# Performance work log

Hardware: AMD Instinct MI355X
Metric: run time of the kernel (lower is better)

Reference implementation:

```python
import jax, jax.numpy as jnp
import numpy as np

B, N, W = 4, 16384, 4          # batch, npoints, point feature width (xyz + intensity)
M, K = 512, 32                  # nsample keypoints, neighbors per keypoint
DIL = 2.0
NK = int(K * DIL)               # dilated candidate pool
KG = 8                          # knn size inside DGCNN edge-convs
C3 = 256


def _fps(xyz, m):
    """Farthest point sampling. xyz: (B,N,3) -> indices (B,m)."""
    Bb, Nn, _ = xyz.shape
    def step(carry, _):
        mind, cur = carry
        p = jnp.take_along_axis(xyz, cur[:, None, None], axis=1)  # (B,1,3)
        d = jnp.sum((xyz - p) ** 2, axis=-1)                       # (B,N)
        mind = jnp.minimum(mind, d)
        nxt = jnp.argmax(mind, axis=-1).astype(jnp.int32)
        return (mind, nxt), cur
    init = (jnp.full((Bb, Nn), 1e10, xyz.dtype), jnp.zeros((Bb,), jnp.int32))
    _, idx = jax.lax.scan(step, init, None, length=m)
    return jnp.transpose(idx)  # (B,m)


def _edge_conv(x, w, g, b, kg):
    """Dynamic-graph edge conv. x: (G,P,C) -> (G,P,D). Feature = cat(x_j-x_i, x_i)."""
    sq = jnp.sum(x * x, axis=-1)
    d2 = sq[:, :, None] + sq[:, None, :] - 2.0 * jnp.einsum('gpc,gqc->gpq', x, x)
    _, idx = jax.lax.top_k(-d2, kg)                                   # (G,P,kg)
    xj = jnp.take_along_axis(x[:, None], idx[..., None], axis=2)      # (G,P,kg,C)
    ef = jnp.concatenate([xj - x[:, :, None, :],
                          jnp.broadcast_to(x[:, :, None, :], xj.shape)], axis=-1)
    h = jnp.einsum('gpkc,cd->gpkd', ef, w)
    h = jax.nn.relu(g * h + b)  # BN (inference, unit running stats) + ReLU
    return jnp.max(h, axis=2)   # max over graph neighbors


def setup_inputs() -> dict:
    key = jax.random.key(0)
    ks = jax.random.split(key, 12)
    s = 0.05
    inp = {
        'x': jax.random.normal(ks[0], (B, N, W), jnp.float32),
        'rand_idx': jax.random.randint(ks[1], (K,), 0, NK),
        # DGCNN edge-conv params
        'w_e1': jax.random.normal(ks[2], (24, 64), jnp.float32) * s,
        'g1': jnp.ones((64,), jnp.float32), 'b1': jnp.zeros((64,), jnp.float32),
        'w_e2': jax.random.normal(ks[3], (128, C3), jnp.float32) * s,
        'g2': jnp.ones((C3,), jnp.float32), 'b2': jnp.zeros((C3,), jnp.float32),
        # saliency MLP (1x1 conv1d stacks)
        'w_m1': jax.random.normal(ks[4], (C3, C3), jnp.float32) * s,
        'bm1': jnp.zeros((C3,), jnp.float32),
        'gm1': jnp.ones((C3,), jnp.float32), 'bbm1': jnp.zeros((C3,), jnp.float32),
        'w_m2': jax.random.normal(ks[5], (C3, C3), jnp.float32) * s,
        'bm2': jnp.zeros((C3,), jnp.float32),
        'gm2': jnp.ones((C3,), jnp.float32), 'bbm2': jnp.zeros((C3,), jnp.float32),
        'w_m3': jax.random.normal(ks[6], (C3, 1), jnp.float32) * s,
        'bm3': jnp.zeros((1,), jnp.float32),
    }
    return inp


def reference(x, rand_idx, w_e1, g1, b1, w_e2, g2, b2,
              w_m1, bm1, gm1, bbm1, w_m2, bm2, gm2, bbm2, w_m3, bm3):
    rand_idx = rand_idx.astype(jnp.int32)
    # ---- FPS keypoint sampling ----
    node_idx = _fps(x[:, :, :3], M)                                   # (B,M)
    node = jnp.take_along_axis(x, node_idx[:, :, None], axis=1)       # (B,M,W)
    # ---- random dilation encoding: nk-NN then random k of them ----
    nxyz, pxyz = node[:, :, :3], x[:, :, :3]
    d2 = (jnp.sum(nxyz * nxyz, -1)[:, :, None] + jnp.sum(pxyz * pxyz, -1)[:, None, :]
          - 2.0 * jnp.einsum('bmc,bnc->bmn', nxyz, pxyz))             # (B,M,N)
    _, nn = jax.lax.top_k(-d2, NK)                                    # (B,M,NK)
    sel = nn[:, :, rand_idx]                                          # (B,M,K)
    neigh = jnp.take_along_axis(x[:, None], sel[..., None], axis=2)   # (B,M,K,W)
    rel = neigh[..., :3] - nxyz[:, :, None, :]
    dist = jnp.linalg.norm(rel, axis=-1, keepdims=True)
    node_rep = jnp.broadcast_to(node[:, :, None, :], neigh.shape)
    cluster = jnp.concatenate([node_rep, neigh, rel, dist], axis=-1)  # (B,M,K,12)
    random_cluster = jnp.transpose(cluster, (0, 3, 1, 2))             # (B,12,M,K)
    random_xyz = neigh[..., :3]                                       # (B,M,K,3)
    # ---- DGCNN embedding per cluster ----
    g = cluster.reshape(B * M, K, 12)
    h = _edge_conv(g, w_e1, g1, b1, KG)                               # (BM,K,64)
    h = _edge_conv(h, w_e2, g2, b2, KG)                               # (BM,K,256)
    emb = jnp.transpose(h.reshape(B, M, K, C3), (0, 3, 1, 2))         # (B,256,M,K)
    # ---- attention-weighted pooling ----
    x1 = jnp.max(emb, axis=1)                                         # (B,M,K)
    aw = jax.nn.softmax(x1, axis=-1)
    keypoints = jnp.einsum('bmk,bmkc->bcm', aw, random_xyz)           # (B,3,M)
    afm = emb * aw[:, None]                                           # (B,256,M,K)
    gcf = jnp.sum(afm, axis=-1)                                       # (B,256,M)
    # ---- saliency uncertainty MLP ----
    h = jax.nn.relu(gm1[None, :, None] * (jnp.einsum('bcm,cd->bdm', gcf, w_m1)
                                          + bm1[None, :, None]) + bbm1[None, :, None])
    h = jax.nn.relu(gm2[None, :, None] * (jnp.einsum('bcm,cd->bdm', h, w_m2)
                                          + bm2[None, :, None]) + bbm2[None, :, None])
    s = jnp.einsum('bcm,cd->bdm', h, w_m3) + bm3[None, :, None]       # (B,1,M)
    sal = jax.nn.softplus(s)[:, 0, :] + 0.001                         # (B,M)
    return keypoints, sal, random_cluster, afm
```

## Files before the change

### kernel.cpp

```cpp
#include <hip/hip_runtime.h>
#include <cstdint>

#define Bn 4
#define Nn 16384
#define Mn 512
#define Kn 32

#define O_SAL 6144
#define O_RC  8192
#define O_AFM 794624

__device__ __forceinline__ unsigned fkey(float f) {
  unsigned b = __float_as_uint(f);
  return (b & 0x80000000u) ? ~b : (b | 0x80000000u);
}

__device__ __forceinline__ unsigned long long dkey(double d) {
  unsigned long long b = (unsigned long long)__double_as_longlong(d);
  return (b & 0x8000000000000000ull) ? ~b : (b | 0x8000000000000000ull);
}

__global__ __launch_bounds__(256) void sq_kernel(const float* __restrict__ x,
                                                 float* __restrict__ sqp) {
#pragma clang fp contract(off)
  int i = blockIdx.x * 256 + threadIdx.x;
  float4 v = ((const float4*)x)[i];
  float qx = v.x * v.x;
  float qy = v.y * v.y;
  float qz = v.z * v.z;
  sqp[i] = (qx + qy) + qz;
}

template <int CTRL>
__device__ __forceinline__ float dppmaxf(float v) {
  int m = __builtin_amdgcn_update_dpp(__float_as_int(v), __float_as_int(v),
                                      CTRL, 0xf, 0xf, false);
  return fmaxf(v, __int_as_float(m));
}

__global__ __launch_bounds__(1024)
__attribute__((amdgpu_waves_per_eu(4, 4)))
void fps_kernel(const float* __restrict__ x, float* __restrict__ node) {
#pragma clang fp contract(off)
  const int b = blockIdx.x;
  const int t = threadIdx.x;
  const float4* xb = (const float4*)(x + (size_t)b * Nn * 4);
  float px[16], py[16], pz[16], mind[16];
  const int base = t * 16;
#pragma unroll
  for (int i = 0; i < 16; ++i) {
    float4 v = xb[base + i];
    px[i] = v.x; py[i] = v.y; pz[i] = v.z;
    mind[i] = 1e10f;
  }
  __shared__ __align__(16) unsigned long long kkey[2][16];
  float cx, cy, cz;
  {
    float4 v = xb[0];
    cx = v.x; cy = v.y; cz = v.z;
    if (t == 0) ((float4*)node)[b * Mn] = v;
  }
  for (int s = 1; s < Mn; ++s) {
#pragma unroll
    for (int i = 0; i < 16; ++i) {
      float dx = px[i] - cx;
      float dy = py[i] - cy;
      float dz = pz[i] - cz;
      float qx = dx * dx;
      float qy = dy * dy;
      float qz = dz * dz;
      float d = (qx + qy) + qz;
      mind[i] = fminf(mind[i], d);
    }
    float a0 = fmaxf(mind[0], mind[1]);
    float a1 = fmaxf(mind[2], mind[3]);
    float a2 = fmaxf(mind[4], mind[5]);
    float a3 = fmaxf(mind[6], mind[7]);
    float a4 = fmaxf(mind[8], mind[9]);
    float a5 = fmaxf(mind[10], mind[11]);
    float a6 = fmaxf(mind[12], mind[13]);
    float a7 = fmaxf(mind[14], mind[15]);
    float b0 = fmaxf(a0, a1);
    float b1 = fmaxf(a2, a3);
    float b2 = fmaxf(a4, a5);
    float b3 = fmaxf(a6, a7);
    float bv = fmaxf(fmaxf(b0, b1), fmaxf(b2, b3));
    int isel = 0;
#pragma unroll
    for (int i = 15; i >= 0; --i)
      if (mind[i] == bv) isel = i;
    float r = bv;
    r = dppmaxf<0x111>(r);
    r = dppmaxf<0x112>(r);
    r = dppmaxf<0x114>(r);
    r = dppmaxf<0x118>(r);
    r = dppmaxf<0x142>(r);
    r = dppmaxf<0x143>(r);
    float wmax = __int_as_float(__builtin_amdgcn_readlane(__float_as_int(r), 63));
    unsigned long long ball = __ballot(bv == wmax);
    int wl = __ffsll(ball) - 1;
    int widx = __builtin_amdgcn_readlane(base + isel, wl);
    if ((t & 63) == 0) {
      unsigned long long key =
          ((unsigned long long)(__float_as_uint(wmax) | 0x80000000u) << 32) |
          (unsigned)(~widx);
      kkey[s & 1][t >> 6] = key;
    }
    __syncthreads();
    {
      unsigned long long kk = kkey[s & 1][t & 15];
#pragma unroll
      for (int off = 1; off < 16; off <<= 1) {
        unsigned long long ok = __shfl_xor(kk, off, 16);
        kk = ok > kk ? ok : kk;
      }
      int wi = __builtin_amdgcn_readfirstlane((int)(~(unsigned)(kk & 0xFFFFFFFFu)));
      float4 nv = xb[wi];
      cx = nv.x; cy = nv.y; cz = nv.z;
      if (t == 0) ((float4*)node)[b * Mn + s] = nv;
    }
  }
}

__global__ __launch_bounds__(256) void knn_kernel(const float* __restrict__ x,
                                                  const float* __restrict__ node,
                                                  const float* __restrict__ sqp,
                                                  const int* __restrict__ rand_idx,
                                                  int* __restrict__ sel) {
#pragma clang fp contract(off)
  const int bm = blockIdx.x;
  const int b = bm >> 9;
  const int t = threadIdx.x;
  const float4* xb = (const float4*)(x + (size_t)b * Nn * 4);
  const float* sq_b = sqp + b * Nn;
  float4 nd = ((const float4*)node)[bm];
  const float nx = nd.x, ny = nd.y, nz = nd.z;
  const float sqmf = (nx * nx + ny * ny) + nz * nz;
  unsigned key[64];
#pragma unroll
  for (int i = 0; i < 64; ++i) {
    int n = t + (i << 8);
    float4 v = xb[n];
    float dot = nx * v.x;
    dot = __builtin_fmaf(ny, v.y, dot);
    dot = __builtin_fmaf(nz, v.z, dot);
    float d2 = (sqmf + sq_b[n]) - 2.0f * dot;
    key[i] = fkey(d2);
  }
  __shared__ unsigned hist[256];
  __shared__ unsigned gsum[16];
  __shared__ unsigned sh_prefix;
  __shared__ int sh_r;
  unsigned prefix = 0, pmask = 0;
  int r = 95;
  for (int shift = 24; shift >= 0; shift -= 8) {
    hist[t] = 0;
    __syncthreads();
#pragma unroll
    for (int i = 0; i < 64; ++i) {
      if ((key[i] & pmask) == prefix) atomicAdd(&hist[(key[i] >> shift) & 255], 1u);
    }
    __syncthreads();
    if (t < 16) {
      unsigned ssum = 0;
#pragma unroll
      for (int j = 0; j < 16; ++j) ssum += hist[t * 16 + j];
      gsum[t] = ssum;
    }
    __syncthreads();
    if (t == 0) {
      int rr = r;
      unsigned g = 0;
      for (unsigned j = 0; j < 16; ++j) {
        int c = (int)gsum[j];
        if (rr < c) { g = j; break; }
        rr -= c;
      }
      unsigned bin = g * 16;
      for (unsigned j = 0; j < 16; ++j) {
        int c = (int)hist[g * 16 + j];
        if (rr < c) { bin = g * 16 + j; break; }
        rr -= c;
      }
      sh_prefix = prefix | (bin << shift);
      sh_r = rr;
    }
    __syncthreads();
    prefix = sh_prefix;
    r = sh_r;
    pmask |= (0xFFu << shift);
  }
  const unsigned T = prefix;
  __shared__ int cnt;
  __shared__ unsigned long long karr[128];
  if (t == 0) cnt = 0;
  __syncthreads();
#pragma unroll
  for (int i = 0; i < 64; ++i) {
    if (key[i] <= T) {
      int pos = atomicAdd(&cnt, 1);
      if (pos < 128) {
        unsigned n = (unsigned)(t + (i << 8));
        karr[pos] = ((unsigned long long)key[i] << 32) | n;
      }
    }
  }
  __syncthreads();
  const int nc = cnt < 128 ? cnt : 128;
  if (t < 128 && t >= nc) karr[t] = ~0ull;
  for (int k = 2; k <= 128; k <<= 1) {
    for (int j = k >> 1; j > 0; j >>= 1) {
      __syncthreads();
      if (t < 64) {
        int i = ((t & ~(j - 1)) << 1) | (t & (j - 1));
        int ip = i | j;
        unsigned long long ka = karr[i], kb = karr[ip];
        bool asc = ((i & k) == 0);
        if ((ka > kb) == asc) { karr[i] = kb; karr[ip] = ka; }
      }
    }
  }
  __syncthreads();
  if (t < 32) {
    int ri = rand_idx[t];
    sel[bm * 32 + t] = (int)(unsigned)(karr[ri] & 0xFFFFFFFFu);
  }
}

__device__ __forceinline__ void topk8(const unsigned long long* row, unsigned char* nb) {
  unsigned long long bk[8];
  unsigned char bi[8];
#pragma unroll
  for (int k = 0; k < 8; ++k) { bk[k] = ~0ull; bi[k] = 255; }
  for (int q = 0; q < 32; ++q) {
    unsigned long long kv = row[q];
    if (kv < bk[7]) {
      bk[7] = kv; bi[7] = (unsigned char)q;
#pragma unroll
      for (int k = 6; k >= 0; --k) {
        if (bk[k + 1] < bk[k]) {
          unsigned long long tk = bk[k]; bk[k] = bk[k + 1]; bk[k + 1] = tk;
          unsigned char ti = bi[k]; bi[k] = bi[k + 1]; bi[k + 1] = ti;
        }
      }
    }
  }
#pragma unroll
  for (int k = 0; k < 8; ++k) nb[k] = bi[k];
}

__global__ __launch_bounds__(256) void group_kernel(
    const float* __restrict__ x, const float* __restrict__ node,
    const int* __restrict__ sel, const float* __restrict__ w_e1,
    const float* __restrict__ g1, const float* __restrict__ b1,
    const float* __restrict__ w_e2, const float* __restrict__ g2,
    const float* __restrict__ b2, float* __restrict__ out,
    float* __restrict__ gcf) {
#pragma clang fp contract(off)
  const int bm = blockIdx.x;
  const int b = bm >> 9;
  const int m = bm & 511;
  const int t = threadIdx.x;

  __shared__ float cl[32][13];
  __shared__ float h1t[64][36];
  __shared__ float h1p[32][68];
  __shared__ unsigned char nbr[32][8];
  __shared__ double sqs[32];
  __shared__ float part[4][32];
  __shared__ float aws[32];
  __shared__ union U {
    struct {
      unsigned long long keys[32][32];
      float we_a[12][64];
      float we_d[12][64];
      float a1[32][65];
      float cd1[32][65];
    } s;
    float a2[32 * 256];
  } u;

  const float4* xb = (const float4*)(x + (size_t)b * Nn * 4);
  const float4 ndv = ((const float4*)node)[bm];

  if (t < 32) {
    int n = sel[bm * 32 + t];
    float4 v = xb[n];
    float rx = v.x - ndv.x;
    float ry = v.y - ndv.y;
    float rz = v.z - ndv.z;
    float ds = (rx * rx + ry * ry) + rz * rz;
    ds = __fsqrt_rn(ds);
    cl[t][0] = ndv.x; cl[t][1] = ndv.y; cl[t][2] = ndv.z; cl[t][3] = ndv.w;
    cl[t][4] = v.x;   cl[t][5] = v.y;   cl[t][6] = v.z;   cl[t][7] = v.w;
    cl[t][8] = rx;    cl[t][9] = ry;    cl[t][10] = rz;   cl[t][11] = ds;
  }
  for (int i = t; i < 768; i += 256) {
    int row = i >> 6, d = i & 63;
    float wa = w_e1[row * 64 + d];
    float wb = w_e1[(row + 12) * 64 + d];
    u.s.we_a[row][d] = wa;
    u.s.we_d[row][d] = wb - wa;
  }
  __syncthreads();

  for (int i = t; i < 384; i += 256) {
    int c = i >> 5, p = i & 31;
    out[O_RC + (((size_t)(b * 12 + c) * 512) + m) * 32 + p] = cl[p][c];
  }
  if (t < 32) {
    double q[12];
#pragma unroll
    for (int c = 0; c < 12; ++c) {
      double cv = (double)cl[t][c];
      q[c] = cv * cv;
    }
    double s01 = q[0] + q[1];
    double s23 = q[2] + q[3];
    double s45 = q[4] + q[5];
    double s67 = q[6] + q[7];
    double s = (s01 + s23) + (s45 + s67);
    s = s + q[8];
    s = s + q[9];
    s = s + q[10];
    s = s + q[11];
    sqs[t] = s;
  }
  __syncthreads();

  {
    int p = t >> 3, q0 = (t & 7) << 2;
#pragma unroll
    for (int qq = 0; qq < 4; ++qq) {
      int q = q0 + qq;
      double dot = 0.0;
#pragma unroll
      for (int c = 0; c < 12; ++c)
        dot = dot + (double)cl[p][c] * (double)cl[q][c];
      double d2 = (sqs[p] + sqs[q]) - 2.0 * dot;
      u.s.keys[p][q] = dkey(d2);
    }
  }
  __syncthreads();

  if (t < 32) topk8(&u.s.keys[t][0], &nbr[t][0]);
  {
    int d = t & 63, pg = (t >> 6) << 3;
#pragma unroll
    for (int pp = 0; pp < 8; ++pp) {
      int p = pg + pp;
      float aA = 0.f, aD = 0.f;
#pragma unroll
      for (int c = 0; c < 12; ++c) {
        float xv = cl[p][c];
        aA = fmaf(xv, u.s.we_a[c][d], aA);
        aD = fmaf(xv, u.s.we_d[c][d], aD);
      }
      u.s.a1[p][d] = aA;
      u.s.cd1[p][d] = aD;
    }
  }
  __syncthreads();

  {
    int d = t & 63, pg = (t >> 6) << 3;
    float g1v = g1[d], b1v = b1[d];
#pragma unroll
    for (int pp = 0; pp < 8; ++pp) {
      int p = pg + pp;
      float cd = u.s.cd1[p][d];
      float hm = -1e30f;
#pragma unroll
      for (int k = 0; k < 8; ++k) {
        int j = nbr[p][k];
        float hv = fmaf(g1v, u.s.a1[j][d] + cd, b1v);
        hv = fmaxf(hv, 0.f);
        hm = fmaxf(hm, hv);
      }
      h1t[d][p] = hm;
      h1p[p][d] = hm;
    }
  }
  __syncthreads();

  if (t < 32) {
    double r[8];
#pragma unroll
    for (int j = 0; j < 8; ++j) {
      double hv = (double)h1p[t][j];
      r[j] = hv * hv;
    }
#pragma unroll
    for (int blk = 1; blk < 8; ++blk) {
#pragma unroll
      for (int j = 0; j < 8; ++j) {
        double hv = (double)h1p[t][blk * 8 + j];
        r[j] = r[j] + hv * hv;
      }
    }
    double s01 = r[0] + r[1];
    double s23 = r[2] + r[3];
    double s45 = r[4] + r[5];
    double s67 = r[6] + r[7];
    sqs[t] = (s01 + s23) + (s45 + s67);
  }
  __syncthreads();

  {
    int p = t >> 3, q0 = (t & 7) << 2;
#pragma unroll
    for (int qq = 0; qq < 4; ++qq) {
      int q = q0 + qq;
      double dot = 0.0;
      for (int c = 0; c < 64; ++c)
        dot = dot + (double)h1p[p][c] * (double)h1p[q][c];
      double d2 = (sqs[p] + sqs[q]) - 2.0 * dot;
      u.s.keys[p][q] = dkey(d2);
    }
  }
  __syncthreads();

  if (t < 32) topk8(&u.s.keys[t][0], &nbr[t][0]);
  __syncthreads();

  float accD[32];
  float embv[32];
  {
    float accA[32];
#pragma unroll
    for (int p = 0; p < 32; ++p) { accA[p] = 0.f; accD[p] = 0.f; }
    for (int c = 0; c < 64; ++c) {
      float wt = w_e2[c * 256 + t];
      float wb = w_e2[(c + 64) * 256 + t];
      float wd = wb - wt;
      const float4* row = (const float4*)&h1t[c][0];
#pragma unroll
      for (int p4 = 0; p4 < 8; ++p4) {
        float4 hv = row[p4];
        accA[4 * p4 + 0] = fmaf(hv.x, wt, accA[4 * p4 + 0]);
        accA[4 * p4 + 1] = fmaf(hv.y, wt, accA[4 * p4 + 1]);
        accA[4 * p4 + 2] = fmaf(hv.z, wt, accA[4 * p4 + 2]);
        accA[4 * p4 + 3] = fmaf(hv.w, wt, accA[4 * p4 + 3]);
        accD[4 * p4 + 0] = fmaf(hv.x, wd, accD[4 * p4 + 0]);
        accD[4 * p4 + 1] = fmaf(hv.y, wd, accD[4 * p4 + 1]);
        accD[4 * p4 + 2] = fmaf(hv.z, wd, accD[4 * p4 + 2]);
        accD[4 * p4 + 3] = fmaf(hv.w, wd, accD[4 * p4 + 3]);
      }
    }
#pragma unroll
    for (int p = 0; p < 32; ++p) u.a2[p * 256 + t] = accA[p];
  }
  __syncthreads();
  {
    float g2v = g2[t], b2v = b2[t];
#pragma unroll
    for (int p = 0; p < 32; ++p) {
      float cd = accD[p];
      float e = -1e30f;
#pragma unroll
      for (int k = 0; k < 8; ++k) {
        int j = nbr[p][k];
        float hv = fmaf(g2v, u.a2[j * 256 + t] + cd, b2v);
        hv = fmaxf(hv, 0.f);
        e = fmaxf(e, hv);
      }
      embv[p] = e;
    }
  }

#pragma unroll
  for (int p = 0; p < 32; ++p) {
    float v = embv[p];
#pragma unroll
    for (int off = 32; off > 0; off >>= 1) v = fmaxf(v, __shfl_xor(v, off));
    if ((t & 63) == 0) part[t >> 6][p] = v;
  }
  __syncthreads();

  if (t < 32) {
    float x1 = fmaxf(fmaxf(part[0][t], part[1][t]), fmaxf(part[2][t], part[3][t]));
    float mx = x1;
#pragma unroll
    for (int off = 16; off > 0; off >>= 1) mx = fmaxf(mx, __shfl_xor(mx, off));
    float ex = expf(x1 - mx);
    float sm = ex;
#pragma unroll
    for (int off = 16; off > 0; off >>= 1) sm += __shfl_xor(sm, off);
    float aw = ex / sm;
    aws[t] = aw;
#pragma unroll
    for (int c = 0; c < 3; ++c) {
      float kv = aw * cl[t][4 + c];
#pragma unroll
      for (int off = 16; off > 0; off >>= 1) kv += __shfl_xor(kv, off);
      if (t == 0) out[((size_t)(b * 3 + c)) * 512 + m] = kv;
    }
  }
  __syncthreads();

  {
    float gsum = 0.f;
    size_t abase = (size_t)O_AFM + (((size_t)(b * 256 + t)) * 512 + m) * 32;
    float4* ap = (float4*)(out + abase);
#pragma unroll
    for (int p4 = 0; p4 < 8; ++p4) {
      float4 o;
      o.x = embv[4 * p4 + 0] * aws[4 * p4 + 0];
      o.y = embv[4 * p4 + 1] * aws[4 * p4 + 1];
      o.z = embv[4 * p4 + 2] * aws[4 * p4 + 2];
      o.w = embv[4 * p4 + 3] * aws[4 * p4 + 3];
      gsum += o.x; gsum += o.y; gsum += o.z; gsum += o.w;
      ap[p4] = o;
    }
    gcf[((size_t)(b * 256 + t)) * 512 + m] = gsum;
  }
}

__global__ __launch_bounds__(256) void mlp_kernel(
    const float* __restrict__ gcf, const float* __restrict__ w_m1,
    const float* __restrict__ bm1, const float* __restrict__ gm1,
    const float* __restrict__ bbm1, const float* __restrict__ w_m2,
    const float* __restrict__ bm2, const float* __restrict__ gm2,
    const float* __restrict__ bbm2, const float* __restrict__ w_m3,
    const float* __restrict__ bm3, float* __restrict__ out) {
  const int blk = blockIdx.x;
  const int b = blk >> 4;
  const int m0 = (blk & 15) << 5;
  const int t = threadIdx.x;
  __shared__ float sbuf[256 * 36];

#pragma unroll
  for (int i = 0; i < 32; ++i) {
    int c = (t >> 5) + (i << 3);
    int j = t & 31;
    sbuf[c * 36 + j] = gcf[((size_t)(b * 256 + c)) * 512 + m0 + j];
  }
  __syncthreads();

  float acc[32];
#pragma unroll
  for (int j = 0; j < 32; ++j) acc[j] = 0.f;
  for (int c = 0; c < 256; ++c) {
    float wv = w_m1[c * 256 + t];
    const float4* row = (const float4*)&sbuf[c * 36];
#pragma unroll
    for (int j4 = 0; j4 < 8; ++j4) {
      float4 g4 = row[j4];
      acc[4 * j4 + 0] = fmaf(g4.x, wv, acc[4 * j4 + 0]);
      acc[4 * j4 + 1] = fmaf(g4.y, wv, acc[4 * j4 + 1]);
      acc[4 * j4 + 2] = fmaf(g4.z, wv, acc[4 * j4 + 2]);
      acc[4 * j4 + 3] = fmaf(g4.w, wv, acc[4 * j4 + 3]);
    }
  }
  float y[32];
  {
    float gv = gm1[t], bv = bm1[t], bbv = bbm1[t];
#pragma unroll
    for (int j = 0; j < 32; ++j) y[j] = fmaxf(fmaf(gv, acc[j] + bv, bbv), 0.f);
  }
  __syncthreads();
#pragma unroll
  for (int j = 0; j < 32; ++j) sbuf[t * 36 + j] = y[j];
  __syncthreads();

#pragma unroll
  for (int j = 0; j < 32; ++j) acc[j] = 0.f;
  for (int c = 0; c < 256; ++c) {
    float wv = w_m2[c * 256 + t];
    const float4* row = (const float4*)&sbuf[c * 36];
#pragma unroll
    for (int j4 = 0; j4 < 8; ++j4) {
      float4 g4 = row[j4];
      acc[4 * j4 + 0] = fmaf(g4.x, wv, acc[4 * j4 + 0]);
      acc[4 * j4 + 1] = fmaf(g4.y, wv, acc[4 * j4 + 1]);
      acc[4 * j4 + 2] = fmaf(g4.z, wv, acc[4 * j4 + 2]);
      acc[4 * j4 + 3] = fmaf(g4.w, wv, acc[4 * j4 + 3]);
    }
  }
  {
    float gv = gm2[t], bv = bm2[t], bbv = bbm2[t];
#pragma unroll
    for (int j = 0; j < 32; ++j) y[j] = fmaxf(fmaf(gv, acc[j] + bv, bbv), 0.f);
  }
  __syncthreads();
  {
    float w3v = w_m3[t];
#pragma unroll
    for (int j = 0; j < 32; ++j) sbuf[t * 36 + j] = y[j] * w3v;
  }
  __syncthreads();
  if (t < 32) {
    float s = 0.f;
    for (int d = 0; d < 256; ++d) s += sbuf[d * 36 + t];
    s += bm3[0];
    float sal = log1pf(expf(-fabsf(s))) + fmaxf(s, 0.f) + 0.001f;
    out[O_SAL + (size_t)b * 512 + m0 + t] = sal;
  }
}

extern "C" void kernel_launch(void* const* d_in, const int* in_sizes, int n_in,
                              void* d_out, int out_size, void* d_ws, size_t ws_size,
                              hipStream_t stream) {
  (void)in_sizes; (void)n_in; (void)out_size; (void)ws_size;
  const float* x = (const float*)d_in[0];
  const int* rand_idx = (const int*)d_in[1];
  const float* w_e1 = (const float*)d_in[2];
  const float* g1 = (const float*)d_in[3];
  const float* b1 = (const float*)d_in[4];
  const float* w_e2 = (const float*)d_in[5];
  const float* g2 = (const float*)d_in[6];
  const float* b2 = (const float*)d_in[7];
  const float* w_m1 = (const float*)d_in[8];
  const float* bm1 = (const float*)d_in[9];
  const float* gm1 = (const float*)d_in[10];
  const float* bbm1 = (const float*)d_in[11];
  const float* w_m2 = (const float*)d_in[12];
  const float* bm2 = (const float*)d_in[13];
  const float* gm2 = (const float*)d_in[14];
  const float* bbm2 = (const float*)d_in[15];
  const float* w_m3 = (const float*)d_in[16];
  const float* bm3 = (const float*)d_in[17];
  float* out = (float*)d_out;
  char* ws = (char*)d_ws;

  float* node = (float*)ws;
  float* sqp = (float*)(ws + 32768);
  int* sel = (int*)(ws + 32768 + 262144);
  float* gcf = (float*)(ws + 32768 + 262144 + 262144);

  sq_kernel<<<256, 256, 0, stream>>>(x, sqp);
  fps_kernel<<<Bn, 1024, 0, stream>>>(x, node);
  knn_kernel<<<Bn * Mn, 256, 0, stream>>>(x, node, sqp, rand_idx, sel);
  group_kernel<<<Bn * Mn, 256, 0, stream>>>(x, node, sel, w_e1, g1, b1, w_e2,
                                            g2, b2, out, gcf);
  mlp_kernel<<<64, 256, 0, stream>>>(gcf, w_m1, bm1, gm1, bbm1, w_m2, bm2, gm2,
                                     bbm2, w_m3, bm3, out);
}
```

Before: 1.623 ms.

## Split farthest point sampling across four blocks per batch with global atomic exchange

FPS now runs on four 1024-thread workgroups per batch instead of one. Each workgroup owns 4096 points and publishes its per-step argmax to a global slot tagged with the step number, then spins until all four slots for that step are written before choosing the next centroid. The aim is to cut per-thread serial work and spread the latency-bound loop over more CUs. In exchange, every step now pays a global-memory round trip. The scheme also depends on all 16 blocks being co-resident, and the slots alias the gcf workspace, which is only safe because FPS finishes before gcf is written.

Result: slower. 1.739 ms (+7.1%).

```diff
diff --git a/kernel.cpp b/kernel.cpp
--- a/kernel.cpp
+++ b/kernel.cpp
@@ -21,9 +21,11 @@
 }
 
 __global__ __launch_bounds__(256) void sq_kernel(const float* __restrict__ x,
-                                                 float* __restrict__ sqp) {
+                                                 float* __restrict__ sqp,
+                                                 unsigned long long* __restrict__ slots) {
 #pragma clang fp contract(off)
   int i = blockIdx.x * 256 + threadIdx.x;
+  if (blockIdx.x == 0 && threadIdx.x < 32) slots[threadIdx.x * 8] = 0ull;
   float4 v = ((const float4*)x)[i];
   float qx = v.x * v.x;
   float qy = v.y * v.y;
@@ -39,30 +41,33 @@
 }
 
 __global__ __launch_bounds__(1024)
-__attribute__((amdgpu_waves_per_eu(4, 4)))
-void fps_kernel(const float* __restrict__ x, float* __restrict__ node) {
+void fps_kernel(const float* __restrict__ x, float* __restrict__ node,
+                unsigned long long* __restrict__ slots) {
 #pragma clang fp contract(off)
-  const int b = blockIdx.x;
+  const int gb = blockIdx.x;
+  const int bb = gb >> 2;
+  const int blk = gb & 3;
   const int t = threadIdx.x;
-  const float4* xb = (const float4*)(x + (size_t)b * Nn * 4);
-  float px[16], py[16], pz[16], mind[16];
-  const int base = t * 16;
-#pragma unroll
-  for (int i = 0; i < 16; ++i) {
+  const float4* xb = (const float4*)(x + (size_t)bb * Nn * 4);
+  float px[4], py[4], pz[4], mind[4];
+  const int base = blk * 4096 + t * 4;
+#pragma unroll
+  for (int i = 0; i < 4; ++i) {
     float4 v = xb[base + i];
     px[i] = v.x; py[i] = v.y; pz[i] = v.z;
     mind[i] = 1e10f;
   }
-  __shared__ __align__(16) unsigned long long kkey[2][16];
+  __shared__ __align__(16) unsigned long long kkey[16];
+  __shared__ unsigned long long rslot[4];
   float cx, cy, cz;
   {
     float4 v = xb[0];
     cx = v.x; cy = v.y; cz = v.z;
-    if (t == 0) ((float4*)node)[b * Mn] = v;
+    if (blk == 0 && t == 0) ((float4*)node)[bb * Mn] = v;
   }
   for (int s = 1; s < Mn; ++s) {
 #pragma unroll
-    for (int i = 0; i < 16; ++i) {
+    for (int i = 0; i < 4; ++i) {
       float dx = px[i] - cx;
       float dy = py[i] - cy;
       float dz = pz[i] - cz;
@@ -72,22 +77,10 @@
       float d = (qx + qy) + qz;
       mind[i] = fminf(mind[i], d);
     }
-    float a0 = fmaxf(mind[0], mind[1]);
-    float a1 = fmaxf(mind[2], mind[3]);
-    float a2 = fmaxf(mind[4], mind[5]);
-    float a3 = fmaxf(mind[6], mind[7]);
-    float a4 = fmaxf(mind[8], mind[9]);
-    float a5 = fmaxf(mind[10], mind[11]);
-    float a6 = fmaxf(mind[12], mind[13]);
-    float a7 = fmaxf(mind[14], mind[15]);
-    float b0 = fmaxf(a0, a1);
-    float b1 = fmaxf(a2, a3);
-    float b2 = fmaxf(a4, a5);
-    float b3 = fmaxf(a6, a7);
-    float bv = fmaxf(fmaxf(b0, b1), fmaxf(b2, b3));
+    float bv = fmaxf(fmaxf(mind[0], mind[1]), fmaxf(mind[2], mind[3]));
     int isel = 0;
 #pragma unroll
-    for (int i = 15; i >= 0; --i)
+    for (int i = 3; i >= 0; --i)
       if (mind[i] == bv) isel = i;
     float r = bv;
     r = dppmaxf<0x111>(r);
@@ -101,23 +94,48 @@
     int wl = __ffsll(ball) - 1;
     int widx = __builtin_amdgcn_readlane(base + isel, wl);
     if ((t & 63) == 0) {
-      unsigned long long key =
+      kkey[t >> 6] =
           ((unsigned long long)(__float_as_uint(wmax) | 0x80000000u) << 32) |
           (unsigned)(~widx);
-      kkey[s & 1][t >> 6] = key;
     }
     __syncthreads();
-    {
-      unsigned long long kk = kkey[s & 1][t & 15];
+    if (t < 64) {
+      unsigned long long kk = kkey[t & 15];
 #pragma unroll
       for (int off = 1; off < 16; off <<= 1) {
         unsigned long long ok = __shfl_xor(kk, off, 16);
         kk = ok > kk ? ok : kk;
       }
-      int wi = __builtin_amdgcn_readfirstlane((int)(~(unsigned)(kk & 0xFFFFFFFFu)));
+      if (t == 0) {
+        unsigned bidx = ~(unsigned)(kk & 0xFFFFFFFFu);
+        unsigned long long v46 = ((kk >> 32) << 14) |
+                                 (unsigned long long)(unsigned)(16383 - (int)bidx);
+        unsigned long long word = ((unsigned long long)s << 46) | v46;
+        __hip_atomic_store(&slots[((s & 1) * 16 + bb * 4 + blk) * 8], word,
+                           __ATOMIC_RELAXED, __HIP_MEMORY_SCOPE_AGENT);
+      }
+      if (t < 4) {
+        unsigned long long vv;
+        do {
+          vv = __hip_atomic_load(&slots[((s & 1) * 16 + bb * 4 + t) * 8],
+                                 __ATOMIC_RELAXED, __HIP_MEMORY_SCOPE_AGENT);
+          if ((vv >> 46) != (unsigned long long)s) __builtin_amdgcn_s_sleep(1);
+        } while ((vv >> 46) != (unsigned long long)s);
+        rslot[t] = vv & ((1ull << 46) - 1);
+      }
+    }
+    __syncthreads();
+    {
+      unsigned long long v0 = rslot[0], v1 = rslot[1];
+      unsigned long long v2 = rslot[2], v3 = rslot[3];
+      unsigned long long va = v0 > v1 ? v0 : v1;
+      unsigned long long vb = v2 > v3 ? v2 : v3;
+      unsigned long long vm = va > vb ? va : vb;
+      int wi = 16383 - (int)(vm & 16383u);
+      wi = __builtin_amdgcn_readfirstlane(wi);
       float4 nv = xb[wi];
       cx = nv.x; cy = nv.y; cz = nv.z;
-      if (t == 0) ((float4*)node)[b * Mn + s] = nv;
+      if (blk == 0 && t == 0) ((float4*)node)[bb * Mn + s] = nv;
     }
   }
 }
@@ -627,9 +645,10 @@
   float* sqp = (float*)(ws + 32768);
   int* sel = (int*)(ws + 32768 + 262144);
   float* gcf = (float*)(ws + 32768 + 262144 + 262144);
-
-  sq_kernel<<<256, 256, 0, stream>>>(x, sqp);
-  fps_kernel<<<Bn, 1024, 0, stream>>>(x, node);
+  unsigned long long* slots = (unsigned long long*)(ws + 32768 + 262144 + 262144);
+
+  sq_kernel<<<256, 256, 0, stream>>>(x, sqp, slots);
+  fps_kernel<<<4 * Bn, 1024, 0, stream>>>(x, node, slots);
   knn_kernel<<<Bn * Mn, 256, 0, stream>>>(x, node, sqp, rand_idx, sel);
   group_kernel<<<Bn * Mn, 256, 0, stream>>>(x, node, sel, w_e1, g1, b1, w_e2,
                                             g2, b2, out, gcf);
```
